# Kernel optimization log

Hardware: AMD Instinct MI355X
Metric: run time of the kernel (lower is better)

The kernel has to match this reference:

```python
import jax, jax.numpy as jnp
import numpy as np

B, C, L, H = 4, 512, 2048, 8
DH = C // H
SCALE = DH ** -0.5
EPS = 1e-5  # torch LayerNorm default


def setup_inputs() -> dict:
    key = jax.random.key(0)
    ks = jax.random.split(key, 3)
    x = jax.random.normal(ks[0], (B, C, L), dtype=jnp.float32)
    # Conv1d kernel_size=1 == per-position linear; weights ~ N(0, 1/C)
    w_qkv = jax.random.normal(ks[1], (3 * C, C), dtype=jnp.float32) / np.sqrt(C)
    b_qkv = jnp.zeros((3 * C,), dtype=jnp.float32)
    # NOTE: original uses zero_module(proj_out); random weights used here so the
    # baseline is non-trivial for kernel correctness testing.
    w_proj = jax.random.normal(ks[2], (C, C), dtype=jnp.float32) / np.sqrt(C)
    b_proj = jnp.zeros((C,), dtype=jnp.float32)
    ln_gamma = jnp.ones((C,), dtype=jnp.float32)
    ln_beta = jnp.zeros((C,), dtype=jnp.float32)
    return {"x": x, "ln_gamma": ln_gamma, "ln_beta": ln_beta,
            "w_qkv": w_qkv, "b_qkv": b_qkv, "w_proj": w_proj, "b_proj": b_proj}


def reference(x, ln_gamma, ln_beta, w_qkv, b_qkv, w_proj, b_proj):
    # ChannelNorm: LayerNorm over channel dim. Work in [B, L, C] layout.
    h = jnp.swapaxes(x, 1, 2)                      # [B, L, C]
    mu = jnp.mean(h, axis=-1, keepdims=True)
    var = jnp.mean((h - mu) ** 2, axis=-1, keepdims=True)
    hn = (h - mu) * jax.lax.rsqrt(var + EPS) * ln_gamma + ln_beta

    # QKV 1x1 conv as GEMM: [B, L, 3C]
    qkv = jnp.einsum('blc,dc->bld', hn, w_qkv) + b_qkv
    qkv = qkv.reshape(B, L, 3, H, DH)
    q, k, v = (qkv[:, :, i].transpose(0, 2, 1, 3) for i in range(3))  # [B, H, L, DH]

    # Scaled dot-product attention (full O(L^2) scores, as in source)
    w = jnp.einsum('bhqd,bhkd->bhqk', q, k) * SCALE
    w = jax.nn.softmax(w, axis=-1)
    o = jnp.einsum('bhqk,bhkd->bhqd', w, v)        # [B, H, L, DH]
    o = o.transpose(0, 2, 1, 3).reshape(B, L, C)

    # proj_out 1x1 conv + residual (dropout in eval mode = identity)
    out = jnp.einsum('blc,dc->bld', o, w_proj) + b_proj
    return jnp.swapaxes(out, 1, 2) + x             # [B, C, L]
```

## Files before the change

### kernel.cpp

```cpp
#include <hip/hip_runtime.h>
#include <hip/hip_bf16.h>

typedef __bf16 bf16;
typedef bf16 bf16x8 __attribute__((ext_vector_type(8)));
typedef bf16 bf16x4 __attribute__((ext_vector_type(4)));
typedef float f32x4 __attribute__((ext_vector_type(4)));

constexpr int B = 4, C = 512, L = 2048, H = 8, DH = 64;
constexpr int BL = B * L;
constexpr int BH = B * H;
constexpr int N_QKV = 3 * C;
constexpr float QSCALE = 0.125f * 1.44269504088896f;
constexpr float EPS = 1e-5f;

constexpr size_t SZ = (size_t)BL * C;
constexpr size_t OFF_HN    = 0;
constexpr size_t OFF_WQKV  = OFF_HN    + SZ * 2;
constexpr size_t OFF_WPROJ = OFF_WQKV  + (size_t)N_QKV * C * 2;
constexpr size_t OFF_Q     = OFF_WPROJ + (size_t)C * C * 2;
constexpr size_t OFF_K     = OFF_Q     + SZ * 2;
constexpr size_t OFF_V     = OFF_K     + SZ * 2;
constexpr size_t OFF_O     = OFF_V     + SZ * 2;
constexpr size_t OFF_STATS = OFF_O     + SZ * 2;
constexpr size_t OFF_OPART = OFF_STATS + (size_t)BL * 2 * 4;
constexpr size_t OFF_ML    = OFF_OPART + (size_t)2 * BH * L * DH * 2;

__device__ __forceinline__ bf16x8 ld8(const bf16* p) {
  return *(const bf16x8*)p;
}

__device__ __forceinline__ void gll16(const bf16* g, bf16* l) {
  __builtin_amdgcn_global_load_lds(
      (const __attribute__((address_space(1))) unsigned int*)(const void*)g,
      (__attribute__((address_space(3))) unsigned int*)(void*)l, 16, 0, 0);
}

__device__ __forceinline__ unsigned pack_bf16(float a, float b) {
  unsigned ua = __builtin_bit_cast(unsigned, a) + 0x8000u;
  unsigned ub = __builtin_bit_cast(unsigned, b) + 0x8000u;
  return __builtin_amdgcn_perm(ub, ua, 0x07060302u);
}
__device__ __forceinline__ float bf_lo(unsigned u) { return __builtin_bit_cast(float, u << 16); }
__device__ __forceinline__ float bf_hi(unsigned u) { return __builtin_bit_cast(float, u & 0xFFFF0000u); }

__global__ __launch_bounds__(1024) void k_ln(const float* __restrict__ x,
                                             const float* __restrict__ gamma,
                                             const float* __restrict__ beta,
                                             const float* __restrict__ wqkv,
                                             const float* __restrict__ wproj,
                                             bf16* __restrict__ hn,
                                             bf16* __restrict__ wqkv_b,
                                             bf16* __restrict__ wproj_b) {
  int blk = blockIdx.x;
  int b = blk >> 6;
  int l0 = (blk & 63) << 5;
  int t = threadIdx.x;
  int ll = t & 31;
  int cg = t >> 5;
  __shared__ float tile[512][33];
  __shared__ float sh_s[32][33];
  __shared__ float sh_q[32][33];
  __shared__ float mu_s[32], rs_s[32];
  const float* xp = x + ((size_t)b * C) * L + l0;
  float s = 0.f, ss = 0.f;
#pragma unroll
  for (int r = 0; r < 16; ++r) {
    int c = cg * 16 + r;
    float v = xp[(size_t)c * L + ll];
    tile[c][ll] = v;
    s += v; ss += v * v;
  }
  sh_s[cg][ll] = s; sh_q[cg][ll] = ss;
  __syncthreads();
  if (t < 32) {
    float ts = 0.f, tq = 0.f;
#pragma unroll
    for (int i = 0; i < 32; ++i) { ts += sh_s[i][t]; tq += sh_q[i][t]; }
    float mu = ts * (1.0f / C);
    float var = tq * (1.0f / C) - mu * mu;
    mu_s[t] = mu;
    rs_s[t] = rsqrtf(var + EPS);
  }
  __syncthreads();
  int c2 = (t & 255) * 2;
  int lgrp = t >> 8;
  float g0 = gamma[c2], g1 = gamma[c2 + 1];
  float b0 = beta[c2],  b1 = beta[c2 + 1];
#pragma unroll
  for (int it = 0; it < 8; ++it) {
    int l = lgrp * 8 + it;
    float mu = mu_s[l], rstd = rs_s[l];
    float v0 = (tile[c2][l]     - mu) * rstd * g0 + b0;
    float v1 = (tile[c2 + 1][l] - mu) * rstd * g1 + b1;
    *(unsigned*)&hn[(size_t)(b * L + l0 + l) * C + c2] = pack_bf16(v0, v1);
  }
  int gid = blk * 1024 + t;
#pragma unroll
  for (int i = 0; i < 3; ++i)
    wqkv_b[gid + i * 262144] = (bf16)wqkv[gid + i * 262144];
  wproj_b[gid] = (bf16)wproj[gid];
}

__global__ __launch_bounds__(256) void k_gemm_qkv(const bf16* __restrict__ hn,
                                                  const bf16* __restrict__ wq,
                                                  const float* __restrict__ bq,
                                                  bf16* __restrict__ qg,
                                                  bf16* __restrict__ kg,
                                                  bf16* __restrict__ vg) {
  int i0 = blockIdx.x;
  int xcd = i0 & 7, slot = i0 >> 3;
  int g = slot / 12, nt = slot - g * 12;
  int mt = g * 8 + xcd;
  int m0 = mt << 7, n0 = nt << 7;
  int t = threadIdx.x, lane = t & 63, w = t >> 6;
  int mw = w >> 1, nw = w & 1;
  int q4 = lane >> 4, c16 = lane & 15;
  __shared__ __align__(16) char smem[36864];
  bf16* As = (bf16*)smem;
  bf16* Bs = (bf16*)(smem + 16384);

  int goff[4], ldsoff[4];
#pragma unroll
  for (int p = 0; p < 4; ++p) {
    int idx = (p * 4 + w) * 64 + lane;
    int row = idx >> 3, s0 = idx & 7;
    goff[p] = row * C + (s0 ^ (row & 7)) * 8;
    ldsoff[p] = (p * 4 + w) * 512;
  }

  f32x4 acc[4][4];
#pragma unroll
  for (int mi = 0; mi < 4; ++mi)
#pragma unroll
    for (int ni = 0; ni < 4; ++ni) acc[mi][ni] = (f32x4){0.f, 0.f, 0.f, 0.f};

  const bf16* ap = hn + (size_t)m0 * C;
  const bf16* bp = wq + (size_t)n0 * C;
  for (int k0 = 0; k0 < C; k0 += 64) {
    __syncthreads();
#pragma unroll
    for (int p = 0; p < 4; ++p) {
      gll16(ap + k0 + goff[p], As + ldsoff[p]);
      gll16(bp + k0 + goff[p], Bs + ldsoff[p]);
    }
    __syncthreads();
#pragma unroll
    for (int kk2 = 0; kk2 < 2; ++kk2) {
      bf16x8 af[4], bfr[4];
#pragma unroll
      for (int mi = 0; mi < 4; ++mi) {
        int row = mw * 64 + mi * 16 + c16;
        af[mi] = ld8(As + row * 64 + ((kk2 * 4 + q4) ^ (row & 7)) * 8);
      }
#pragma unroll
      for (int ni = 0; ni < 4; ++ni) {
        int row = nw * 64 + ni * 16 + c16;
        bfr[ni] = ld8(Bs + row * 64 + ((kk2 * 4 + q4) ^ (row & 7)) * 8);
      }
#pragma unroll
      for (int mi = 0; mi < 4; ++mi)
#pragma unroll
        for (int ni = 0; ni < 4; ++ni)
          acc[mi][ni] = __builtin_amdgcn_mfma_f32_16x16x32_bf16(af[mi], bfr[ni], acc[mi][ni], 0, 0, 0);
    }
  }
  __syncthreads();

  int i = nt >> 2;
  int h = ((nt & 3) << 1) + nw;
  int b = m0 >> 11;
  int l0 = (m0 & (L - 1)) + mw * 64;
  float bias[4];
#pragma unroll
  for (int ni = 0; ni < 4; ++ni) bias[ni] = bq[n0 + nw * 64 + ni * 16 + c16];
  bf16* Os = (bf16*)(smem + w * 9216);

  if (i == 2) {
#pragma unroll
    for (int mi = 0; mi < 4; ++mi)
#pragma unroll
      for (int ni = 0; ni < 4; ++ni) {
        bf16x4 pk;
#pragma unroll
        for (int r = 0; r < 4; ++r) pk[r] = (bf16)(acc[mi][ni][r] + bias[ni]);
        *(bf16x4*)&Os[(ni * 16 + c16) * 72 + mi * 16 + q4 * 4] = pk;
      }
    __syncthreads();
    const bf16* src = Os + lane * 72;
    bf16* dst = vg + ((size_t)((b * H + h) * DH + lane)) * L + l0;
#pragma unroll
    for (int s = 0; s < 8; ++s)
      *(uint4*)(dst + s * 8) = *(const uint4*)(src + s * 8);
  } else {
    float sc = (i == 0) ? QSCALE : 1.0f;
#pragma unroll
    for (int mi = 0; mi < 4; ++mi)
#pragma unroll
      for (int ni = 0; ni < 4; ++ni)
#pragma unroll
        for (int r = 0; r < 4; ++r)
          Os[(mi * 16 + q4 * 4 + r) * 72 + ni * 16 + c16] = (bf16)((acc[mi][ni][r] + bias[ni]) * sc);
    __syncthreads();
    bf16* dst0 = (i == 0) ? qg : kg;
    const bf16* src = Os + lane * 72;
    bf16* dst = dst0 + ((size_t)((b * H + h) * L + l0 + lane)) * DH;
#pragma unroll
    for (int s = 0; s < 8; ++s)
      *(uint4*)(dst + s * 8) = *(const uint4*)(src + s * 8);
  }
}

__global__ __launch_bounds__(256, 4) void k_attn(const bf16* __restrict__ qg,
                                                 const bf16* __restrict__ kg,
                                                 const bf16* __restrict__ vt,
                                                 bf16* __restrict__ opart,
                                                 float* __restrict__ lsum) {
  int i0 = blockIdx.x;
  int x = i0 & 7, slot = i0 >> 3;
  int bh = ((slot >> 5) << 3) + x;
  int inner = slot & 31;
  int js = inner >> 4;
  int qt = inner & 15;
  int t = threadIdx.x, lane = t & 63, w = t >> 6;
  int q4 = lane >> 4, c16 = lane & 15;
  __shared__ __align__(16) bf16 Ks[2][64][64];
  __shared__ __align__(16) bf16 Vts[2][64][64];
  const bf16* qptr  = qg + ((size_t)bh * L + qt * 128 + w * 32) * DH;
  const bf16* kptr  = kg + (size_t)bh * L * DH;
  const bf16* vtptr = vt + (size_t)bh * DH * L;

  int ksoff[2], vsoff[2];
#pragma unroll
  for (int p = 0; p < 2; ++p) {
    int ci = p * 256 + w * 64 + lane;
    int row = ci >> 3, s0 = ci & 7;
    int ch = s0 ^ (row & 7);
    ksoff[p] = row * DH + ch * 8;
    vsoff[p] = row * L + ch * 8;
  }
  int sw = c16 & 7;

  bf16x8 qf[2][2];
#pragma unroll
  for (int qb = 0; qb < 2; ++qb)
#pragma unroll
    for (int kk2 = 0; kk2 < 2; ++kk2)
      qf[qb][kk2] = ld8(&qptr[(size_t)(qb * 16 + c16) * DH + kk2 * 32 + q4 * 8]);

  f32x4 o_acc[2][4];
  float l_i[2] = {0.f, 0.f};
#pragma unroll
  for (int qb = 0; qb < 2; ++qb)
#pragma unroll
    for (int db = 0; db < 4; ++db) o_acc[qb][db] = (f32x4){0.f, 0.f, 0.f, 0.f};

  {
    int j0 = js * 1024;
#pragma unroll
    for (int p = 0; p < 2; ++p) {
      gll16(kptr + (size_t)j0 * DH + ksoff[p], &Ks[0][0][0]  + (p * 4 + w) * 512);
      gll16(vtptr + j0 + vsoff[p],             &Vts[0][0][0] + (p * 4 + w) * 512);
    }
  }
  asm volatile("s_waitcnt vmcnt(0)" ::: "memory");
  __builtin_amdgcn_s_barrier();
  __builtin_amdgcn_sched_barrier(0);

  for (int it = 0; it < 16; ++it) {
    int cur = it & 1;
    if (it < 15) {
      int j1 = js * 1024 + (it + 1) * 64;
#pragma unroll
      for (int p = 0; p < 2; ++p) {
        gll16(kptr + (size_t)j1 * DH + ksoff[p], &Ks[cur ^ 1][0][0]  + (p * 4 + w) * 512);
        gll16(vtptr + j1 + vsoff[p],             &Vts[cur ^ 1][0][0] + (p * 4 + w) * 512);
      }
    }
    const bf16* KsC = &Ks[cur][0][0];
    const bf16* VsC = &Vts[cur][0][0];

    f32x4 s[2][4];
#pragma unroll
    for (int qb = 0; qb < 2; ++qb)
#pragma unroll
      for (int jb = 0; jb < 4; ++jb) s[qb][jb] = (f32x4){0.f, 0.f, 0.f, 0.f};
#pragma unroll
    for (int kk2 = 0; kk2 < 2; ++kk2) {
      int choff = ((kk2 * 4 + q4) ^ sw) * 8;
#pragma unroll
      for (int jb = 0; jb < 4; ++jb) {
        bf16x8 kf = ld8(KsC + (jb * 16 + c16) * 64 + choff);
        s[0][jb] = __builtin_amdgcn_mfma_f32_16x16x32_bf16(kf, qf[0][kk2], s[0][jb], 0, 0, 0);
        s[1][jb] = __builtin_amdgcn_mfma_f32_16x16x32_bf16(kf, qf[1][kk2], s[1][jb], 0, 0, 0);
      }
    }

#pragma unroll
    for (int qb = 0; qb < 2; ++qb) {
      float rs = 0.f;
#pragma unroll
      for (int jb = 0; jb < 4; ++jb)
#pragma unroll
        for (int r = 0; r < 4; ++r) {
          float p_ = __builtin_amdgcn_exp2f(s[qb][jb][r]);
          s[qb][jb][r] = p_;
          rs += p_;
        }
      l_i[qb] += rs;
    }

    bf16x8 vf[2][4];
#pragma unroll
    for (int kk2 = 0; kk2 < 2; ++kk2) {
      int choff = ((kk2 * 4 + q4) ^ sw) * 8;
#pragma unroll
      for (int db = 0; db < 4; ++db)
        vf[kk2][db] = ld8(VsC + (db * 16 + c16) * 64 + choff);
    }

#pragma unroll
    for (int qb = 0; qb < 2; ++qb) {
#pragma unroll
      for (int kk2 = 0; kk2 < 2; ++kk2) {
        unsigned a = pack_bf16(s[qb][2 * kk2][0],     s[qb][2 * kk2][1]);
        unsigned b = pack_bf16(s[qb][2 * kk2][2],     s[qb][2 * kk2][3]);
        unsigned c = pack_bf16(s[qb][2 * kk2 + 1][0], s[qb][2 * kk2 + 1][1]);
        unsigned d = pack_bf16(s[qb][2 * kk2 + 1][2], s[qb][2 * kk2 + 1][3]);
        asm("v_permlane32_swap_b32 %0, %1" : "+v"(a), "+v"(c));
        asm("v_permlane32_swap_b32 %0, %1" : "+v"(b), "+v"(d));
        asm("v_permlane16_swap_b32 %0, %1" : "+v"(a), "+v"(c));
        asm("v_permlane16_swap_b32 %0, %1" : "+v"(b), "+v"(d));
        uint4 pu = {a, b, c, d};
        bf16x8 pf = __builtin_bit_cast(bf16x8, pu);
#pragma unroll
        for (int db = 0; db < 4; ++db)
          o_acc[qb][db] = __builtin_amdgcn_mfma_f32_16x16x32_bf16(vf[kk2][db], pf, o_acc[qb][db], 0, 0, 0);
      }
    }

    asm volatile("s_waitcnt vmcnt(0)" ::: "memory");
    __builtin_amdgcn_s_barrier();
    __builtin_amdgcn_sched_barrier(0);
  }

#pragma unroll
  for (int qb = 0; qb < 2; ++qb) {
    float lf = l_i[qb];
    lf += __shfl_xor(lf, 16, 64);
    lf += __shfl_xor(lf, 32, 64);
    int q = qt * 128 + w * 32 + qb * 16 + c16;
    bf16* op = opart + (((size_t)js * BH + bh) * L + q) * DH;
#pragma unroll
    for (int db = 0; db < 4; ++db) {
      uint2 pk;
      pk.x = pack_bf16(o_acc[qb][db][0], o_acc[qb][db][1]);
      pk.y = pack_bf16(o_acc[qb][db][2], o_acc[qb][db][3]);
      *(uint2*)&op[db * 16 + q4 * 4] = pk;
    }
    if (q4 == 0) lsum[((size_t)js * BH + bh) * L + q] = lf;
  }
}

__global__ __launch_bounds__(256) void k_gemm_proj(const bf16* __restrict__ opart,
                                                   const float* __restrict__ lsum,
                                                   const bf16* __restrict__ wp,
                                                   const float* __restrict__ bp,
                                                   const float* __restrict__ x,
                                                   float* __restrict__ out) {
  int i0 = blockIdx.x;
  int xcd = i0 & 7, slot = i0 >> 3;
  int nt = slot & 7, g = slot >> 3;
  int mt = g * 8 + xcd;
  int m0 = mt << 6, n0 = nt << 6;
  int t = threadIdx.x;
  int lane = t & 63, w = t >> 6;
  int q4 = lane >> 4, c16 = lane & 15;
  __shared__ __align__(16) bf16 As[64][72];
  __shared__ __align__(16) bf16 Bs[64][72];
  __shared__ float Ot[64][65];
  __shared__ float invs[64][9];
  int b = m0 >> 11, q0 = m0 & (L - 1);
  for (int i = t; i < 512; i += 256) {
    int row = i >> 3, h = i & 7;
    int bhh = b * 8 + h;
    float l0v = lsum[(size_t)bhh * L + q0 + row];
    float l1v = lsum[((size_t)BH + bhh) * L + q0 + row];
    invs[row][h] = 1.0f / (l0v + l1v);
  }
  f32x4 acc[4];
#pragma unroll
  for (int nb = 0; nb < 4; ++nb) acc[nb] = (f32x4){0.f, 0.f, 0.f, 0.f};

  for (int k0 = 0; k0 < C; k0 += 64) {
    __syncthreads();
    int h = k0 >> 6;
    const bf16* ap0 = opart + ((size_t)(b * 8 + h) * L + q0) * 64;
    const bf16* ap1 = opart + ((size_t)(BH + b * 8 + h) * L + q0) * 64;
#pragma unroll
    for (int p = 0; p < 2; ++p) {
      int idx = p * 256 + t;
      int row = idx >> 3, ch = idx & 7;
      uint4 u0 = *(const uint4*)(ap0 + (size_t)row * 64 + ch * 8);
      uint4 u1 = *(const uint4*)(ap1 + (size_t)row * 64 + ch * 8);
      float inv = invs[row][h];
      unsigned* pu0 = (unsigned*)&u0;
      unsigned* pu1 = (unsigned*)&u1;
      uint4 m;
      unsigned* pm = (unsigned*)&m;
#pragma unroll
      for (int k = 0; k < 4; ++k)
        pm[k] = pack_bf16((bf_lo(pu0[k]) + bf_lo(pu1[k])) * inv,
                          (bf_hi(pu0[k]) + bf_hi(pu1[k])) * inv);
      *(uint4*)&As[row][ch * 8] = m;
      *(bf16x8*)&Bs[row][ch * 8] = ld8(&wp[(size_t)(n0 + row) * C + k0 + ch * 8]);
    }
    __syncthreads();
#pragma unroll
    for (int kk = 0; kk < 64; kk += 32) {
      bf16x8 a = ld8(&As[w * 16 + c16][kk + q4 * 8]);
#pragma unroll
      for (int nb = 0; nb < 4; ++nb) {
        bf16x8 bfr = ld8(&Bs[nb * 16 + c16][kk + q4 * 8]);
        acc[nb] = __builtin_amdgcn_mfma_f32_16x16x32_bf16(a, bfr, acc[nb], 0, 0, 0);
      }
    }
  }
  __syncthreads();
#pragma unroll
  for (int nb = 0; nb < 4; ++nb)
#pragma unroll
    for (int r = 0; r < 4; ++r)
      Ot[w * 16 + q4 * 4 + r][nb * 16 + c16] = acc[nb][r];
  __syncthreads();
#pragma unroll
  for (int r = 0; r < 16; ++r) {
    int cl = w * 16 + r;
    int c = n0 + cl;
    size_t idx = (size_t)(b * C + c) * L + q0 + lane;
    out[idx] = Ot[lane][cl] + bp[c] + x[idx];
  }
}

extern "C" void kernel_launch(void* const* d_in, const int* in_sizes, int n_in,
                              void* d_out, int out_size, void* d_ws, size_t ws_size,
                              hipStream_t stream) {
  const float* x     = (const float*)d_in[0];
  const float* gamma = (const float*)d_in[1];
  const float* beta  = (const float*)d_in[2];
  const float* wqkv  = (const float*)d_in[3];
  const float* bqkv  = (const float*)d_in[4];
  const float* wproj = (const float*)d_in[5];
  const float* bproj = (const float*)d_in[6];
  float* out = (float*)d_out;
  char* ws = (char*)d_ws;
  bf16* hn  = (bf16*)(ws + OFF_HN);
  bf16* wqb = (bf16*)(ws + OFF_WQKV);
  bf16* wpb = (bf16*)(ws + OFF_WPROJ);
  bf16* qbp = (bf16*)(ws + OFF_Q);
  bf16* kbp = (bf16*)(ws + OFF_K);
  bf16* vbp = (bf16*)(ws + OFF_V);
  bf16* opart = (bf16*)(ws + OFF_OPART);
  float* lsum = (float*)(ws + OFF_ML);

  hipLaunchKernelGGL(k_ln, dim3(B * (L / 32)), dim3(1024), 0, stream,
                     x, gamma, beta, wqkv, wproj, hn, wqb, wpb);
  hipLaunchKernelGGL(k_gemm_qkv, dim3((BL / 128) * (N_QKV / 128)), dim3(256), 0, stream,
                     hn, wqb, bqkv, qbp, kbp, vbp);
  hipLaunchKernelGGL(k_attn, dim3(B * H * (L / 128) * 2), dim3(256), 0, stream,
                     qbp, kbp, vbp, opart, lsum);
  hipLaunchKernelGGL(k_gemm_proj, dim3((BL / 64) * (C / 64)), dim3(256), 0, stream,
                     opart, lsum, wpb, bproj, x, out);
}
```

Before: 170.2 us.

## Double-buffer LDS tiles in QKV and projection GEMMs with K-step of 32

Both the QKV GEMM and the output projection GEMM switch from single-buffered 64-wide K tiles to double-buffered 32-wide K tiles. The next tile's global loads are issued before the current tile's MFMAs, so memory latency overlaps compute, and each iteration needs one barrier instead of two. The QKV kernel gets a new XOR swizzle for 32-element rows, and the projection kernel prefetches into registers before the merge-and-normalize step. The cost is twice as many loop iterations with less MFMA work per barrier, and the overlap in the QKV kernel relies on the async gll16 loads not being waited on too early.

New measurement: 168.7 us. Within noise of the previous version (-0.8%).

```diff
diff --git a/kernel.cpp b/kernel.cpp
--- a/kernel.cpp
+++ b/kernel.cpp
@@ -119,13 +119,14 @@
   bf16* As = (bf16*)smem;
   bf16* Bs = (bf16*)(smem + 16384);
 
-  int goff[4], ldsoff[4];
-#pragma unroll
-  for (int p = 0; p < 4; ++p) {
-    int idx = (p * 4 + w) * 64 + lane;
-    int row = idx >> 3, s0 = idx & 7;
-    goff[p] = row * C + (s0 ^ (row & 7)) * 8;
-    ldsoff[p] = (p * 4 + w) * 512;
+  int goff[2], ldsoff[2];
+#pragma unroll
+  for (int p = 0; p < 2; ++p) {
+    int idx = p * 256 + t;
+    int row = idx >> 2, s0 = idx & 3;
+    int key = (row + (row >> 2)) & 3;
+    goff[p] = row * C + ((s0 ^ key) * 8);
+    ldsoff[p] = idx * 8;
   }
 
   f32x4 acc[4][4];
@@ -136,35 +137,46 @@
 
   const bf16* ap = hn + (size_t)m0 * C;
   const bf16* bp = wq + (size_t)n0 * C;
-  for (int k0 = 0; k0 < C; k0 += 64) {
+
+#pragma unroll
+  for (int p = 0; p < 2; ++p) {
+    gll16(ap + goff[p], As + ldsoff[p]);
+    gll16(bp + goff[p], Bs + ldsoff[p]);
+  }
+  __syncthreads();
+
+  for (int it = 0; it < 16; ++it) {
+    int cur = it & 1;
+    if (it < 15) {
+      int k1 = (it + 1) * 32;
+#pragma unroll
+      for (int p = 0; p < 2; ++p) {
+        gll16(ap + k1 + goff[p], As + (cur ^ 1) * 4096 + ldsoff[p]);
+        gll16(bp + k1 + goff[p], Bs + (cur ^ 1) * 4096 + ldsoff[p]);
+      }
+    }
+    const bf16* Ac = As + cur * 4096;
+    const bf16* Bc = Bs + cur * 4096;
+    bf16x8 af[4], bfr[4];
+#pragma unroll
+    for (int mi = 0; mi < 4; ++mi) {
+      int row = mw * 64 + mi * 16 + c16;
+      int key = (row + (row >> 2)) & 3;
+      af[mi] = ld8(Ac + row * 32 + ((q4 ^ key) * 8));
+    }
+#pragma unroll
+    for (int ni = 0; ni < 4; ++ni) {
+      int row = nw * 64 + ni * 16 + c16;
+      int key = (row + (row >> 2)) & 3;
+      bfr[ni] = ld8(Bc + row * 32 + ((q4 ^ key) * 8));
+    }
+#pragma unroll
+    for (int mi = 0; mi < 4; ++mi)
+#pragma unroll
+      for (int ni = 0; ni < 4; ++ni)
+        acc[mi][ni] = __builtin_amdgcn_mfma_f32_16x16x32_bf16(af[mi], bfr[ni], acc[mi][ni], 0, 0, 0);
     __syncthreads();
-#pragma unroll
-    for (int p = 0; p < 4; ++p) {
-      gll16(ap + k0 + goff[p], As + ldsoff[p]);
-      gll16(bp + k0 + goff[p], Bs + ldsoff[p]);
-    }
-    __syncthreads();
-#pragma unroll
-    for (int kk2 = 0; kk2 < 2; ++kk2) {
-      bf16x8 af[4], bfr[4];
-#pragma unroll
-      for (int mi = 0; mi < 4; ++mi) {
-        int row = mw * 64 + mi * 16 + c16;
-        af[mi] = ld8(As + row * 64 + ((kk2 * 4 + q4) ^ (row & 7)) * 8);
-      }
-#pragma unroll
-      for (int ni = 0; ni < 4; ++ni) {
-        int row = nw * 64 + ni * 16 + c16;
-        bfr[ni] = ld8(Bs + row * 64 + ((kk2 * 4 + q4) ^ (row & 7)) * 8);
-      }
-#pragma unroll
-      for (int mi = 0; mi < 4; ++mi)
-#pragma unroll
-        for (int ni = 0; ni < 4; ++ni)
-          acc[mi][ni] = __builtin_amdgcn_mfma_f32_16x16x32_bf16(af[mi], bfr[ni], acc[mi][ni], 0, 0, 0);
-    }
-  }
-  __syncthreads();
+  }
 
   int i = nt >> 2;
   int h = ((nt & 3) << 1) + nw;
@@ -375,8 +387,8 @@
   int t = threadIdx.x;
   int lane = t & 63, w = t >> 6;
   int q4 = lane >> 4, c16 = lane & 15;
-  __shared__ __align__(16) bf16 As[64][72];
-  __shared__ __align__(16) bf16 Bs[64][72];
+  __shared__ __align__(16) bf16 As[2][64][40];
+  __shared__ __align__(16) bf16 Bs[2][64][40];
   __shared__ float Ot[64][65];
   __shared__ float invs[64][9];
   int b = m0 >> 11, q0 = m0 & (L - 1);
@@ -387,45 +399,63 @@
     float l1v = lsum[((size_t)BH + bhh) * L + q0 + row];
     invs[row][h] = 1.0f / (l0v + l1v);
   }
+  int srow = t >> 2, s0 = t & 3;
   f32x4 acc[4];
 #pragma unroll
   for (int nb = 0; nb < 4; ++nb) acc[nb] = (f32x4){0.f, 0.f, 0.f, 0.f};
 
-  for (int k0 = 0; k0 < C; k0 += 64) {
-    __syncthreads();
-    int h = k0 >> 6;
-    const bf16* ap0 = opart + ((size_t)(b * 8 + h) * L + q0) * 64;
-    const bf16* ap1 = opart + ((size_t)(BH + b * 8 + h) * L + q0) * 64;
-#pragma unroll
-    for (int p = 0; p < 2; ++p) {
-      int idx = p * 256 + t;
-      int row = idx >> 3, ch = idx & 7;
-      uint4 u0 = *(const uint4*)(ap0 + (size_t)row * 64 + ch * 8);
-      uint4 u1 = *(const uint4*)(ap1 + (size_t)row * 64 + ch * 8);
-      float inv = invs[row][h];
-      unsigned* pu0 = (unsigned*)&u0;
-      unsigned* pu1 = (unsigned*)&u1;
+  const bf16* a00 = opart + (((size_t)(b * 8 + 0) * L + q0 + srow)) * 64 + s0 * 8;
+  uint4 u0 = *(const uint4*)a00;
+  uint4 u1 = *(const uint4*)(a00 + (size_t)BH * L * 64);
+  bf16x8 wv = ld8(&wp[(size_t)(n0 + srow) * C + s0 * 8]);
+  __syncthreads();
+  {
+    float inv = invs[srow][0];
+    unsigned* p0 = (unsigned*)&u0;
+    unsigned* p1 = (unsigned*)&u1;
+    uint4 m;
+    unsigned* pm = (unsigned*)&m;
+#pragma unroll
+    for (int k = 0; k < 4; ++k)
+      pm[k] = pack_bf16((bf_lo(p0[k]) + bf_lo(p1[k])) * inv,
+                        (bf_hi(p0[k]) + bf_hi(p1[k])) * inv);
+    *(uint4*)&As[0][srow][s0 * 8] = m;
+    *(bf16x8*)&Bs[0][srow][s0 * 8] = wv;
+  }
+  __syncthreads();
+
+  for (int it = 0; it < 16; ++it) {
+    int cur = it & 1;
+    uint4 n0u, n1u; bf16x8 nwv;
+    if (it < 15) {
+      int s = it + 1;
+      int h = s >> 1;
+      const bf16* a0 = opart + (((size_t)(b * 8 + h) * L + q0 + srow)) * 64 + (s & 1) * 32 + s0 * 8;
+      n0u = *(const uint4*)a0;
+      n1u = *(const uint4*)(a0 + (size_t)BH * L * 64);
+      nwv = ld8(&wp[(size_t)(n0 + srow) * C + s * 32 + s0 * 8]);
+    }
+    bf16x8 a = ld8(&As[cur][w * 16 + c16][q4 * 8]);
+#pragma unroll
+    for (int nb = 0; nb < 4; ++nb) {
+      bf16x8 bfr = ld8(&Bs[cur][nb * 16 + c16][q4 * 8]);
+      acc[nb] = __builtin_amdgcn_mfma_f32_16x16x32_bf16(a, bfr, acc[nb], 0, 0, 0);
+    }
+    if (it < 15) {
+      float inv = invs[srow][(it + 1) >> 1];
+      unsigned* p0 = (unsigned*)&n0u;
+      unsigned* p1 = (unsigned*)&n1u;
       uint4 m;
       unsigned* pm = (unsigned*)&m;
 #pragma unroll
       for (int k = 0; k < 4; ++k)
-        pm[k] = pack_bf16((bf_lo(pu0[k]) + bf_lo(pu1[k])) * inv,
-                          (bf_hi(pu0[k]) + bf_hi(pu1[k])) * inv);
-      *(uint4*)&As[row][ch * 8] = m;
-      *(bf16x8*)&Bs[row][ch * 8] = ld8(&wp[(size_t)(n0 + row) * C + k0 + ch * 8]);
+        pm[k] = pack_bf16((bf_lo(p0[k]) + bf_lo(p1[k])) * inv,
+                          (bf_hi(p0[k]) + bf_hi(p1[k])) * inv);
+      *(uint4*)&As[cur ^ 1][srow][s0 * 8] = m;
+      *(bf16x8*)&Bs[cur ^ 1][srow][s0 * 8] = nwv;
     }
     __syncthreads();
-#pragma unroll
-    for (int kk = 0; kk < 64; kk += 32) {
-      bf16x8 a = ld8(&As[w * 16 + c16][kk + q4 * 8]);
-#pragma unroll
-      for (int nb = 0; nb < 4; ++nb) {
-        bf16x8 bfr = ld8(&Bs[nb * 16 + c16][kk + q4 * 8]);
-        acc[nb] = __builtin_amdgcn_mfma_f32_16x16x32_bf16(a, bfr, acc[nb], 0, 0, 0);
-      }
-    }
-  }
-  __syncthreads();
+  }
 #pragma unroll
   for (int nb = 0; nb < 4; ++nb)
 #pragma unroll
```
